# Optimization experiments

Hardware: AMD Instinct MI355X
Metric: run time of the kernel (lower is better)

## Reference

```python
import jax, jax.numpy as jnp
import numpy as np

B, C, H, W = 8, 128, 64, 64


def setup_inputs() -> dict:
    key = jax.random.key(0)
    ks = jax.random.split(key, 9)
    d = C
    return {
        "x": jax.random.normal(ks[0], (B, C, H, W), dtype=jnp.float32),
        "qw": jax.random.normal(ks[1], (d, d), dtype=jnp.float32),
        "qb": jax.random.normal(ks[2], (d,), dtype=jnp.float32),
        "kw": jax.random.normal(ks[3], (d, d), dtype=jnp.float32),
        "kb": jax.random.normal(ks[4], (d,), dtype=jnp.float32),
        "vw": jax.random.normal(ks[5], (d, d), dtype=jnp.float32),
        "vb": jax.random.normal(ks[6], (d,), dtype=jnp.float32),
        "proj_w": jax.random.normal(ks[7], (d, d), dtype=jnp.float32),
        "proj_b": jax.random.normal(ks[8], (d,), dtype=jnp.float32),
    }


def reference(x, qw, qb, kw, kb, vw, vb, proj_w, proj_b):
    b, c, h, w = x.shape
    n = h * w  # number of spatial tokens
    # permute to channels-last and flatten spatial dims: (b, n, c)
    xt = jnp.transpose(x, (0, 2, 3, 1)).reshape(b, n, c)
    q = xt @ qw + qb
    k = xt @ kw + kb
    v = xt @ vw + vb
    scale = c ** (-0.5)
    # full (n x n) attention over flattened spatial tokens, single head
    attn = jax.nn.softmax(jnp.einsum("bnc,bmc->bnm", q, k) * scale, axis=-1)
    hout = jnp.einsum("bnm,bmc->bnc", attn, v) @ proj_w + proj_b
    out = xt + hout  # residual is on the permuted (channels-last) x, per source
    return out.reshape(b, h, w, c)
```

## Files before the change

### kernel.cpp

```cpp
#include <hip/hip_runtime.h>

#define NB 8
#define CD 128
#define NN 4096
#define SCALE 0.08838834764831845f
#define L2E 1.44269504088896f

typedef __bf16 bf16x8 __attribute__((ext_vector_type(8)));
typedef float f32x4 __attribute__((ext_vector_type(4)));

__device__ __forceinline__ unsigned swz256(unsigned row, unsigned b) {
  unsigned s = b >> 4, o = b & 15u;
  unsigned sw = (s & 8u) | ((s & 7u) ^ (row & 7u));
  return row * 256u + sw * 16u + o;
}
__device__ __forceinline__ unsigned swz128(unsigned row, unsigned b) {
  unsigned s = b >> 4, o = b & 15u;
  unsigned sw = (s ^ row) & 7u;
  return row * 128u + sw * 16u + o;
}

__global__ __launch_bounds__(256, 2) void qkv_kernel(
    const float* __restrict__ x,
    const float* __restrict__ qw, const float* __restrict__ qb,
    const float* __restrict__ kw, const float* __restrict__ kb,
    const float* __restrict__ vw, const float* __restrict__ vb,
    __bf16* __restrict__ Qh, __bf16* __restrict__ Ql,
    __bf16* __restrict__ Kh, __bf16* __restrict__ Kl,
    __bf16* __restrict__ Vt)
{
  __shared__ __align__(16) unsigned char sm[49664];
  const int tid = threadIdx.x;
  const int lane = tid & 63, wv = tid >> 6;
  const int l15 = lane & 15, g = lane >> 4;
  const int b = blockIdx.y;
  const int n0 = blockIdx.x * 64;
  const f32x4 Z4 = {0.f, 0.f, 0.f, 0.f};

  #pragma unroll 4
  for (int i = 0; i < 32; ++i) {
    int e = i * 256 + tid;
    int nl = e & 63, c = e >> 6;
    float f = x[((size_t)(b * CD + c)) * NN + n0 + nl];
    __bf16 h = (__bf16)f;
    __bf16 lo = (__bf16)(f - (float)h);
    unsigned off = swz256((unsigned)nl, (unsigned)(c * 2));
    *(__bf16*)(sm + off) = h;
    *(__bf16*)(sm + 16384 + off) = lo;
  }
  __syncthreads();

  bf16x8 ah[4], al[4];
  #pragma unroll
  for (int kk = 0; kk < 4; ++kk) {
    unsigned off = swz256((unsigned)(wv * 16 + l15), (unsigned)(kk * 64 + g * 16));
    ah[kk] = *(const bf16x8*)(sm + off);
    al[kk] = *(const bf16x8*)(sm + 16384 + off);
  }

  for (int mat = 0; mat < 2; ++mat) {
    const float* gw = mat ? kw : qw;
    const float* gb = mat ? kb : qb;
    __bf16* Oh = mat ? Kh : Qh;
    __bf16* Ol = mat ? Kl : Ql;
    const float sc = mat ? 1.0f : SCALE;
    for (int qd = 0; qd < 4; ++qd) {
      #pragma unroll 4
      for (int i = 0; i < 16; ++i) {
        int e = i * 256 + tid;
        int dl = e & 31, c = e >> 5;
        float f = gw[c * CD + qd * 32 + dl];
        __bf16 h = (__bf16)f;
        __bf16 lo = (__bf16)(f - (float)h);
        unsigned off = swz256((unsigned)dl, (unsigned)(c * 2));
        *(__bf16*)(sm + 32768 + off) = h;
        *(__bf16*)(sm + 40960 + off) = lo;
      }
      __syncthreads();
      #pragma unroll
      for (int fr = 0; fr < 2; ++fr) {
        f32x4 acc = Z4;
        #pragma unroll
        for (int kk = 0; kk < 4; ++kk) {
          unsigned off = swz256((unsigned)(fr * 16 + l15), (unsigned)(kk * 64 + g * 16));
          bf16x8 bh = *(const bf16x8*)(sm + 32768 + off);
          bf16x8 bl = *(const bf16x8*)(sm + 40960 + off);
          acc = __builtin_amdgcn_mfma_f32_16x16x32_bf16(ah[kk], bh, acc, 0, 0, 0);
          acc = __builtin_amdgcn_mfma_f32_16x16x32_bf16(ah[kk], bl, acc, 0, 0, 0);
          acc = __builtin_amdgcn_mfma_f32_16x16x32_bf16(al[kk], bh, acc, 0, 0, 0);
        }
        const int dout = qd * 32 + fr * 16 + l15;
        const float bias = gb[dout];
        #pragma unroll
        for (int r = 0; r < 4; ++r) {
          int row = n0 + wv * 16 + g * 4 + r;
          float v = (acc[r] + bias) * sc;
          __bf16 h = (__bf16)v;
          __bf16 lo = (__bf16)(v - (float)h);
          size_t go = ((size_t)(b * NN + row)) * CD + dout;
          Oh[go] = h;
          Ol[go] = lo;
        }
      }
      __syncthreads();
    }
  }

  f32x4 accV[8];
  #pragma unroll
  for (int i = 0; i < 8; ++i) accV[i] = Z4;
  for (int qd = 0; qd < 4; ++qd) {
    #pragma unroll 4
    for (int i = 0; i < 16; ++i) {
      int e = i * 256 + tid;
      int dl = e & 31, c = e >> 5;
      float f = vw[c * CD + qd * 32 + dl];
      *(__bf16*)(sm + 32768 + swz256((unsigned)dl, (unsigned)(c * 2))) = (__bf16)f;
    }
    __syncthreads();
    #pragma unroll
    for (int fr = 0; fr < 2; ++fr) {
      f32x4 acc = accV[qd * 2 + fr];
      #pragma unroll
      for (int kk = 0; kk < 4; ++kk) {
        unsigned off = swz256((unsigned)(fr * 16 + l15), (unsigned)(kk * 64 + g * 16));
        bf16x8 bh = *(const bf16x8*)(sm + 32768 + off);
        acc = __builtin_amdgcn_mfma_f32_16x16x32_bf16(ah[kk], bh, acc, 0, 0, 0);
      }
      accV[qd * 2 + fr] = acc;
    }
    __syncthreads();
  }
  #pragma unroll
  for (int df = 0; df < 8; ++df) {
    int dout = df * 16 + l15;
    float bias = vb[dout];
    #pragma unroll
    for (int r = 0; r < 4; ++r) {
      int row = wv * 16 + g * 4 + r;
      *(__bf16*)(sm + 32768 + (row * 132 + dout) * 2) = (__bf16)(accV[df][r] + bias);
    }
  }
  __syncthreads();
  #pragma unroll 4
  for (int i = 0; i < 32; ++i) {
    int e = i * 256 + tid;
    int nl = e & 63, dout = e >> 6;
    __bf16 v = *(const __bf16*)(sm + 32768 + (nl * 132 + dout) * 2);
    Vt[((size_t)(b * CD + dout)) * NN + n0 + nl] = v;
  }
}

__global__ __launch_bounds__(256, 2) void attn_kernel(
    const __bf16* __restrict__ Qh, const __bf16* __restrict__ Ql,
    const __bf16* __restrict__ Kh, const __bf16* __restrict__ Kl,
    const __bf16* __restrict__ Vt, const float* __restrict__ x,
    const float* __restrict__ pw, const float* __restrict__ pb,
    float* __restrict__ out)
{
  __shared__ __align__(16) unsigned char sm[57344];
  const int tid = threadIdx.x;
  const int lane = tid & 63, wv = tid >> 6;
  const int l15 = lane & 15, g = lane >> 4;
  const int b = blockIdx.y;
  const int q0 = blockIdx.x * 64;
  const f32x4 Z4 = {0.f, 0.f, 0.f, 0.f};

  bf16x8 qh[4], ql[4];
  #pragma unroll
  for (int kk = 0; kk < 4; ++kk) {
    size_t off = ((size_t)(b * NN + q0 + wv * 16 + l15)) * CD + kk * 32 + g * 8;
    qh[kk] = *(const bf16x8*)(Qh + off);
    ql[kk] = *(const bf16x8*)(Ql + off);
  }

  f32x4 accO[8];
  #pragma unroll
  for (int i = 0; i < 8; ++i) accO[i] = Z4;
  float mrow[4], lrow[4];
  #pragma unroll
  for (int r = 0; r < 4; ++r) { mrow[r] = -__builtin_inff(); lrow[r] = 0.f; }

  for (int kt = 0; kt < 64; ++kt) {
    const int kbase = b * NN + kt * 64;
    #pragma unroll
    for (int i = 0; i < 4; ++i) {
      int id = i * 256 + tid;
      int r = id >> 4, s = id & 15;
      size_t go = ((size_t)(kbase + r)) * CD + s * 8;
      unsigned off = swz256((unsigned)r, (unsigned)(s * 16));
      *(bf16x8*)(sm + off) = *(const bf16x8*)(Kh + go);
      *(bf16x8*)(sm + 16384 + off) = *(const bf16x8*)(Kl + go);
      int r2 = id >> 3, s2 = id & 7;
      *(bf16x8*)(sm + 32768 + swz128((unsigned)r2, (unsigned)(s2 * 16))) =
          *(const bf16x8*)(Vt + ((size_t)(b * CD + r2)) * NN + kt * 64 + s2 * 8);
    }
    __syncthreads();

    f32x4 s4[4];
    #pragma unroll
    for (int kf = 0; kf < 4; ++kf) s4[kf] = Z4;
    #pragma unroll
    for (int kf = 0; kf < 4; ++kf) {
      #pragma unroll
      for (int kk = 0; kk < 4; ++kk) {
        unsigned off = swz256((unsigned)(kf * 16 + l15), (unsigned)(kk * 64 + g * 16));
        bf16x8 bh = *(const bf16x8*)(sm + off);
        bf16x8 bl = *(const bf16x8*)(sm + 16384 + off);
        s4[kf] = __builtin_amdgcn_mfma_f32_16x16x32_bf16(qh[kk], bh, s4[kf], 0, 0, 0);
        s4[kf] = __builtin_amdgcn_mfma_f32_16x16x32_bf16(qh[kk], bl, s4[kf], 0, 0, 0);
        s4[kf] = __builtin_amdgcn_mfma_f32_16x16x32_bf16(ql[kk], bh, s4[kf], 0, 0, 0);
      }
    }

    float alpha[4];
    #pragma unroll
    for (int r = 0; r < 4; ++r) {
      float mx = fmaxf(fmaxf(s4[0][r], s4[1][r]), fmaxf(s4[2][r], s4[3][r]));
      mx = fmaxf(mx, __shfl_xor(mx, 1));
      mx = fmaxf(mx, __shfl_xor(mx, 2));
      mx = fmaxf(mx, __shfl_xor(mx, 4));
      mx = fmaxf(mx, __shfl_xor(mx, 8));
      float mn = fmaxf(mrow[r], mx);
      alpha[r] = exp2f((mrow[r] - mn) * L2E);
      mrow[r] = mn;
      float ps = 0.f;
      #pragma unroll
      for (int kf = 0; kf < 4; ++kf) {
        float p = exp2f((s4[kf][r] - mn) * L2E);
        s4[kf][r] = p;
        ps += p;
      }
      ps += __shfl_xor(ps, 1);
      ps += __shfl_xor(ps, 2);
      ps += __shfl_xor(ps, 4);
      ps += __shfl_xor(ps, 8);
      lrow[r] = lrow[r] * alpha[r] + ps;
    }

    #pragma unroll
    for (int kf = 0; kf < 4; ++kf) {
      #pragma unroll
      for (int r = 0; r < 4; ++r) {
        unsigned row = (unsigned)(wv * 16 + g * 4 + r);
        *(__bf16*)(sm + 49152 + swz128(row, (unsigned)((kf * 16 + l15) * 2))) =
            (__bf16)s4[kf][r];
      }
    }
    #pragma unroll
    for (int df = 0; df < 8; ++df) {
      #pragma unroll
      for (int r = 0; r < 4; ++r) accO[df][r] *= alpha[r];
    }
    bf16x8 pa[2];
    #pragma unroll
    for (int kk2 = 0; kk2 < 2; ++kk2)
      pa[kk2] = *(const bf16x8*)(sm + 49152 +
                  swz128((unsigned)(wv * 16 + l15), (unsigned)(kk2 * 64 + g * 16)));
    #pragma unroll
    for (int df = 0; df < 8; ++df) {
      #pragma unroll
      for (int kk2 = 0; kk2 < 2; ++kk2) {
        bf16x8 bv = *(const bf16x8*)(sm + 32768 +
                      swz128((unsigned)(df * 16 + l15), (unsigned)(kk2 * 64 + g * 16)));
        accO[df] = __builtin_amdgcn_mfma_f32_16x16x32_bf16(pa[kk2], bv, accO[df], 0, 0, 0);
      }
    }
    __syncthreads();
  }

  float rl[4];
  #pragma unroll
  for (int r = 0; r < 4; ++r) rl[r] = 1.0f / lrow[r];
  #pragma unroll
  for (int df = 0; df < 8; ++df) {
    #pragma unroll
    for (int r = 0; r < 4; ++r) {
      unsigned row = (unsigned)(wv * 16 + g * 4 + r);
      *(__bf16*)(sm + swz256(row, (unsigned)((df * 16 + l15) * 2))) =
          (__bf16)(accO[df][r] * rl[r]);
    }
  }
  #pragma unroll 4
  for (int i = 0; i < 16; ++i) {
    int e = i * 256 + tid;
    int c = e >> 5, d4 = e & 31;
    const float4 w4 = *(const float4*)(pw + c * CD + d4 * 4);
    *(__bf16*)(sm + 16384 + swz256((unsigned)(d4 * 4 + 0), (unsigned)(c * 2))) = (__bf16)w4.x;
    *(__bf16*)(sm + 16384 + swz256((unsigned)(d4 * 4 + 1), (unsigned)(c * 2))) = (__bf16)w4.y;
    *(__bf16*)(sm + 16384 + swz256((unsigned)(d4 * 4 + 2), (unsigned)(c * 2))) = (__bf16)w4.z;
    *(__bf16*)(sm + 16384 + swz256((unsigned)(d4 * 4 + 3), (unsigned)(c * 2))) = (__bf16)w4.w;
  }
  __syncthreads();

  bf16x8 oa[4];
  #pragma unroll
  for (int kk = 0; kk < 4; ++kk)
    oa[kk] = *(const bf16x8*)(sm + swz256((unsigned)(wv * 16 + l15),
                                          (unsigned)(kk * 64 + g * 16)));
  #pragma unroll
  for (int df = 0; df < 8; ++df) {
    f32x4 acc = Z4;
    #pragma unroll
    for (int kk = 0; kk < 4; ++kk) {
      bf16x8 bw = *(const bf16x8*)(sm + 16384 +
                    swz256((unsigned)(df * 16 + l15), (unsigned)(kk * 64 + g * 16)));
      acc = __builtin_amdgcn_mfma_f32_16x16x32_bf16(oa[kk], bw, acc, 0, 0, 0);
    }
    const int cc = df * 16 + l15;
    const float bias = pb[cc];
    #pragma unroll
    for (int r = 0; r < 4; ++r) {
      int row = q0 + wv * 16 + g * 4 + r;
      float val = acc[r] + bias + x[((size_t)(b * CD + cc)) * NN + row];
      out[((size_t)(b * NN + row)) * CD + cc] = val;
    }
  }
}

extern "C" void kernel_launch(void* const* d_in, const int* in_sizes, int n_in,
                              void* d_out, int out_size, void* d_ws, size_t ws_size,
                              hipStream_t stream) {
  (void)in_sizes; (void)n_in; (void)out_size; (void)ws_size;
  const float* x  = (const float*)d_in[0];
  const float* qw = (const float*)d_in[1];
  const float* qb = (const float*)d_in[2];
  const float* kw = (const float*)d_in[3];
  const float* kb = (const float*)d_in[4];
  const float* vw = (const float*)d_in[5];
  const float* vb = (const float*)d_in[6];
  const float* pw = (const float*)d_in[7];
  const float* pb = (const float*)d_in[8];
  float* out = (float*)d_out;

  const size_t SZ = (size_t)NB * NN * CD;
  __bf16* Qh = (__bf16*)d_ws;
  __bf16* Ql = Qh + SZ;
  __bf16* Kh = Ql + SZ;
  __bf16* Kl = Kh + SZ;
  __bf16* Vt = Kl + SZ;

  dim3 grid(NN / 64, NB), blk(256);
  qkv_kernel<<<grid, blk, 0, stream>>>(x, qw, qb, kw, kb, vw, vb,
                                       Qh, Ql, Kh, Kl, Vt);
  attn_kernel<<<grid, blk, 0, stream>>>(Qh, Ql, Kh, Kl, Vt, x, pw, pb, out);
}
```

Baseline: 351.4 us.

## Prefetch next K/V tile into registers and skip rescale when max unchanged

The flash-attention loop now issues global loads for the next K/V tile into registers before computing on the current tile, then commits them to shared memory after the PV matmul, overlapping global latency with MFMA work. Online-softmax rescaling of the accumulator is skipped when no row max grew in the wave. s_setprio hints raise priority around the MFMA blocks. This costs extra registers (12 bf16x8 vectors) and an additional barrier per iteration, which may reduce occupancy.

```diff
diff --git a/kernel.cpp b/kernel.cpp
--- a/kernel.cpp
+++ b/kernel.cpp
@@ -181,25 +181,44 @@
   #pragma unroll
   for (int r = 0; r < 4; ++r) { mrow[r] = -__builtin_inff(); lrow[r] = 0.f; }
 
+  bf16x8 pkh[4], pkl[4], pvv[4];
+  const int rK = tid >> 4, sK = tid & 15;
+  const int rV = tid >> 3, sV = tid & 7;
+
+  #define ISSUE_TILE(KT)                                                        \
+    {                                                                           \
+      const size_t kb_ = (size_t)(b * NN + (KT) * 64);                          \
+      _Pragma("unroll")                                                         \
+      for (int i = 0; i < 4; ++i) {                                             \
+        pkh[i] = *(const bf16x8*)(Kh + (kb_ + i * 16 + rK) * CD + sK * 8);      \
+        pkl[i] = *(const bf16x8*)(Kl + (kb_ + i * 16 + rK) * CD + sK * 8);      \
+        pvv[i] = *(const bf16x8*)(Vt + ((size_t)(b * CD) + i * 32 + rV) * NN +  \
+                                  (KT) * 64 + sV * 8);                          \
+      }                                                                         \
+    }
+  #define COMMIT_TILE()                                                         \
+    {                                                                           \
+      _Pragma("unroll")                                                         \
+      for (int i = 0; i < 4; ++i) {                                             \
+        unsigned o_ = swz256((unsigned)(i * 16 + rK), (unsigned)(sK * 16));     \
+        *(bf16x8*)(sm + o_) = pkh[i];                                           \
+        *(bf16x8*)(sm + 16384 + o_) = pkl[i];                                   \
+        *(bf16x8*)(sm + 32768 +                                                 \
+                   swz128((unsigned)(i * 32 + rV), (unsigned)(sV * 16))) = pvv[i]; \
+      }                                                                         \
+    }
+
+  ISSUE_TILE(0);
+  COMMIT_TILE();
+  __syncthreads();
+
   for (int kt = 0; kt < 64; ++kt) {
-    const int kbase = b * NN + kt * 64;
-    #pragma unroll
-    for (int i = 0; i < 4; ++i) {
-      int id = i * 256 + tid;
-      int r = id >> 4, s = id & 15;
-      size_t go = ((size_t)(kbase + r)) * CD + s * 8;
-      unsigned off = swz256((unsigned)r, (unsigned)(s * 16));
-      *(bf16x8*)(sm + off) = *(const bf16x8*)(Kh + go);
-      *(bf16x8*)(sm + 16384 + off) = *(const bf16x8*)(Kl + go);
-      int r2 = id >> 3, s2 = id & 7;
-      *(bf16x8*)(sm + 32768 + swz128((unsigned)r2, (unsigned)(s2 * 16))) =
-          *(const bf16x8*)(Vt + ((size_t)(b * CD + r2)) * NN + kt * 64 + s2 * 8);
-    }
-    __syncthreads();
+    if (kt < 63) ISSUE_TILE(kt + 1);
 
     f32x4 s4[4];
     #pragma unroll
     for (int kf = 0; kf < 4; ++kf) s4[kf] = Z4;
+    __builtin_amdgcn_s_setprio(1);
     #pragma unroll
     for (int kf = 0; kf < 4; ++kf) {
       #pragma unroll
@@ -212,8 +231,10 @@
         s4[kf] = __builtin_amdgcn_mfma_f32_16x16x32_bf16(ql[kk], bh, s4[kf], 0, 0, 0);
       }
     }
-
-    float alpha[4];
+    __builtin_amdgcn_s_setprio(0);
+
+    float ps[4], mnew[4];
+    bool grow = false;
     #pragma unroll
     for (int r = 0; r < 4; ++r) {
       float mx = fmaxf(fmaxf(s4[0][r], s4[1][r]), fmaxf(s4[2][r], s4[3][r]));
@@ -222,21 +243,32 @@
       mx = fmaxf(mx, __shfl_xor(mx, 4));
       mx = fmaxf(mx, __shfl_xor(mx, 8));
       float mn = fmaxf(mrow[r], mx);
-      alpha[r] = exp2f((mrow[r] - mn) * L2E);
-      mrow[r] = mn;
-      float ps = 0.f;
+      mnew[r] = mn;
+      grow = grow || (mn > mrow[r]);
+      float p0 = 0.f;
       #pragma unroll
       for (int kf = 0; kf < 4; ++kf) {
         float p = exp2f((s4[kf][r] - mn) * L2E);
         s4[kf][r] = p;
-        ps += p;
-      }
-      ps += __shfl_xor(ps, 1);
-      ps += __shfl_xor(ps, 2);
-      ps += __shfl_xor(ps, 4);
-      ps += __shfl_xor(ps, 8);
-      lrow[r] = lrow[r] * alpha[r] + ps;
-    }
+        p0 += p;
+      }
+      p0 += __shfl_xor(p0, 1);
+      p0 += __shfl_xor(p0, 2);
+      p0 += __shfl_xor(p0, 4);
+      p0 += __shfl_xor(p0, 8);
+      ps[r] = p0;
+    }
+    if (__any((int)grow)) {
+      #pragma unroll
+      for (int r = 0; r < 4; ++r) {
+        float alpha = exp2f((mrow[r] - mnew[r]) * L2E);
+        lrow[r] *= alpha;
+        #pragma unroll
+        for (int df = 0; df < 8; ++df) accO[df][r] *= alpha;
+      }
+    }
+    #pragma unroll
+    for (int r = 0; r < 4; ++r) { mrow[r] = mnew[r]; lrow[r] += ps[r]; }
 
     #pragma unroll
     for (int kf = 0; kf < 4; ++kf) {
@@ -247,16 +279,13 @@
             (__bf16)s4[kf][r];
       }
     }
-    #pragma unroll
-    for (int df = 0; df < 8; ++df) {
-      #pragma unroll
-      for (int r = 0; r < 4; ++r) accO[df][r] *= alpha[r];
-    }
+
     bf16x8 pa[2];
     #pragma unroll
     for (int kk2 = 0; kk2 < 2; ++kk2)
       pa[kk2] = *(const bf16x8*)(sm + 49152 +
                   swz128((unsigned)(wv * 16 + l15), (unsigned)(kk2 * 64 + g * 16)));
+    __builtin_amdgcn_s_setprio(1);
     #pragma unroll
     for (int df = 0; df < 8; ++df) {
       #pragma unroll
@@ -266,8 +295,14 @@
         accO[df] = __builtin_amdgcn_mfma_f32_16x16x32_bf16(pa[kk2], bv, accO[df], 0, 0, 0);
       }
     }
+    __builtin_amdgcn_s_setprio(0);
+
     __syncthreads();
-  }
+    if (kt < 63) COMMIT_TILE();
+    __syncthreads();
+  }
+  #undef ISSUE_TILE
+  #undef COMMIT_TILE
 
   float rl[4];
   #pragma unroll
```

Result: no change. 344.6 us (-1.9%).
